# Kernel tuning notes

Hardware: AMD Instinct MI355X
Metric: run time of the kernel (lower is better)

Reference implementation:

```python
import jax, jax.numpy as jnp
import numpy as np

NUM_CAPSULE = 64
DIM_CAPSULE = 128
ROUTINGS = 3
EPS = 1e-7  # K.epsilon()


def squash(s, axis=-1):
    sq_norm = jnp.sum(jnp.square(s), axis=axis, keepdims=True) + EPS
    scale = jnp.sqrt(sq_norm) / (0.5 + sq_norm)
    return scale * s


def setup_inputs() -> dict:
    key = jax.random.key(0)
    k1, k2 = jax.random.split(key)
    B, N_IN, D_IN = 16, 512, 256
    x = jax.random.normal(k1, (B, N_IN, D_IN), dtype=jnp.float32)
    # glorot-uniform kernel (flattened conv1d kernel of shape (1, D_IN, NC*DC))
    fan_out = NUM_CAPSULE * DIM_CAPSULE
    limit = float(np.sqrt(6.0 / (D_IN + fan_out)))
    kernel = jax.random.uniform(k2, (D_IN, fan_out), dtype=jnp.float32,
                                minval=-limit, maxval=limit)
    return {"x": x, "kernel": kernel}


def reference(x, kernel):
    B, N, _ = x.shape
    # conv1d with kernel_size=1 == matmul over last dim
    hat = jnp.einsum('bni,io->bno', x, kernel)
    hat = hat.reshape(B, N, NUM_CAPSULE, DIM_CAPSULE).transpose(0, 2, 1, 3)  # [B, C, N, D]
    b = jnp.zeros((B, NUM_CAPSULE, N), dtype=hat.dtype)
    o = None
    for i in range(ROUTINGS):
        c = jax.nn.softmax(b, axis=1)  # softmax over output capsules (axis 1)
        o = squash(jnp.einsum('bcn,bcnd->bcd', c, hat))  # [B, C, D]
        if i < ROUTINGS - 1:
            b = b + jnp.einsum('bcd,bcnd->bcn', o, hat)
    return o
```

## Files before the change

### kernel.cpp

```cpp
#include <hip/hip_runtime.h>
#include <hip/hip_bf16.h>

#define NB 16
#define NN 512
#define DI 256
#define NC 64
#define ND 128
#define FO 8192
#define NP 16

typedef __attribute__((ext_vector_type(8))) short short8v;
typedef __attribute__((ext_vector_type(4))) short short4v;
typedef __attribute__((ext_vector_type(4))) float f32x4;
typedef unsigned short us16;

__device__ __forceinline__ us16 f2b(float f) {
  union { __hip_bfloat16 h; us16 u; } cv; cv.h = __float2bfloat16(f); return cv.u;
}
__device__ __forceinline__ float b2f(us16 u) {
  union { unsigned u; float f; } cv; cv.u = ((unsigned)u) << 16; return cv.f;
}

__global__ __launch_bounds__(256) void k_pre(const float* __restrict__ x,
                                             const float* __restrict__ kern,
                                             us16* __restrict__ khT,
                                             us16* __restrict__ kh,
                                             us16* __restrict__ xh,
                                             us16* __restrict__ xhT,
                                             float* __restrict__ xsum_p) {
  int task = blockIdx.x;
  int tid = threadIdx.x;

  if (task < 512) {
    int c = task >> 3, i0 = (task & 7) * 32;
    __shared__ float buf[32][129];
#pragma unroll
    for (int k = 0; k < 4; ++k) {
      int e4 = tid + k * 256;
      int r = e4 >> 5, dq = e4 & 31;
      float4 v = *(const float4*)(kern + (size_t)(i0 + r) * FO + c * ND + dq * 4);
      buf[r][dq * 4 + 0] = v.x; buf[r][dq * 4 + 1] = v.y;
      buf[r][dq * 4 + 2] = v.z; buf[r][dq * 4 + 3] = v.w;
    }
    __syncthreads();
#pragma unroll
    for (int k = 0; k < 16; ++k) {
      int e = tid + k * 256;
      int il = e & 31, d = e >> 5;
      khT[((size_t)c * ND + d) * DI + i0 + il] = f2b(buf[il][d]);
    }
  } else if (task < 1024) {
    int idx = task - 512;
    int b = idx >> 5, rem = idx & 31;
    int nb = (rem >> 2) * 64, ib = (rem & 3) * 64;
    __shared__ float buf2[64][68];
#pragma unroll
    for (int k = 0; k < 4; ++k) {
      int e4 = tid + k * 256;
      int nl = e4 >> 4, q4 = e4 & 15;
      float4 v = *(const float4*)(x + ((size_t)b * NN + nb + nl) * DI + ib + q4 * 4);
      *(float4*)&buf2[nl][q4 * 4] = v;
    }
    __syncthreads();
    {
      int nl = tid >> 2, ig = (tid & 3) * 16;
      us16 tmp[16];
#pragma unroll
      for (int e = 0; e < 16; ++e) tmp[e] = f2b(buf2[nl][ig + e]);
      us16* dst = xh + ((size_t)b * NN + nb + nl) * DI + ib + ig;
      *(short8v*)dst = *(short8v*)tmp;
      *(short8v*)(dst + 8) = *(short8v*)(tmp + 8);
    }
    {
      int il = tid & 63, ng = tid >> 6;
      us16 tmp[16];
#pragma unroll
      for (int e = 0; e < 16; ++e) tmp[e] = f2b(buf2[ng * 16 + e][il]);
      us16* dst = xhT + ((size_t)b * DI + ib + il) * NN + nb + ng * 16;
      *(short8v*)dst = *(short8v*)tmp;
      *(short8v*)(dst + 8) = *(short8v*)(tmp + 8);
    }
  } else if (task < 1088) {
    int idx = task - 1024;
    int b = idx >> 2, q = idx & 3;
    int ns = tid >> 6, i4 = tid & 63;
    float4 a = {0.f, 0.f, 0.f, 0.f};
    const float4* xp = (const float4*)(x + ((size_t)b * NN + q * 128 + ns * 32) * DI) + i4;
#pragma unroll 4
    for (int n = 0; n < 32; ++n) {
      float4 v = xp[(size_t)n * 64];
      a.x += v.x; a.y += v.y; a.z += v.z; a.w += v.w;
    }
    __shared__ float4 red[4][64];
    red[ns][i4] = a;
    __syncthreads();
    if (ns == 0) {
      float4 s0 = red[0][i4], s1 = red[1][i4], s2 = red[2][i4], s3 = red[3][i4];
      float4 s;
      s.x = s0.x + s1.x + s2.x + s3.x;  s.y = s0.y + s1.y + s2.y + s3.y;
      s.z = s0.z + s1.z + s2.z + s3.z;  s.w = s0.w + s1.w + s2.w + s3.w;
      ((float4*)(xsum_p + ((size_t)q * NB + b) * DI))[i4] = s;
    }
  } else {
    int blk2 = task - 1088;
#pragma unroll
    for (int t = 0; t < 16; ++t) {
      size_t e = (size_t)blk2 * 16384 + (size_t)t * 1024 + (size_t)tid * 4;
      float4 v = *(const float4*)(kern + e);
      us16 tmp[4] = {f2b(v.x), f2b(v.y), f2b(v.z), f2b(v.w)};
      *(short4v*)(kh + e) = *(short4v*)tmp;
    }
  }
}

template <bool FIRST>
__global__ __launch_bounds__(256) void k_owm(const us16* __restrict__ khT,
                                             const us16* __restrict__ kh,
                                             const us16* __restrict__ yp_in,
                                             const float* __restrict__ xsum_p,
                                             us16* __restrict__ whc) {
  int c = blockIdx.x, b0 = blockIdx.y * 4;
  int tid = threadIdx.x;
  int lane = tid & 63, w = tid >> 6;
  int m16 = lane & 15, ko = lane >> 4;

  __shared__ us16 ybf[16][DI];
  __shared__ float o_f32[4][ND];
  __shared__ us16 ob[4][ND];

  {
    int bb = tid >> 6, i4 = tid & 63;
    float4 v;
    if constexpr (FIRST) {
      float4 s0 = ((const float4*)(xsum_p + ((size_t)0 * NB + b0 + bb) * DI))[i4];
      float4 s1 = ((const float4*)(xsum_p + ((size_t)1 * NB + b0 + bb) * DI))[i4];
      float4 s2 = ((const float4*)(xsum_p + ((size_t)2 * NB + b0 + bb) * DI))[i4];
      float4 s3 = ((const float4*)(xsum_p + ((size_t)3 * NB + b0 + bb) * DI))[i4];
      v.x = (s0.x + s1.x + s2.x + s3.x) * (1.f / 64.f);
      v.y = (s0.y + s1.y + s2.y + s3.y) * (1.f / 64.f);
      v.z = (s0.z + s1.z + s2.z + s3.z) * (1.f / 64.f);
      v.w = (s0.w + s1.w + s2.w + s3.w) * (1.f / 64.f);
    } else {
      float a0 = 0.f, a1 = 0.f, a2 = 0.f, a3 = 0.f;
      const us16* base = yp_in + ((size_t)(b0 + bb) * NC + c) * DI + i4 * 4;
#pragma unroll
      for (int p = 0; p < NP; ++p) {
        short4v t = *(const short4v*)(base + (size_t)p * (NB * NC * DI));
        a0 += b2f((us16)t[0]); a1 += b2f((us16)t[1]);
        a2 += b2f((us16)t[2]); a3 += b2f((us16)t[3]);
      }
      v.x = a0; v.y = a1; v.z = a2; v.w = a3;
    }
    us16 tmp[4] = {f2b(v.x), f2b(v.y), f2b(v.z), f2b(v.w)};
    *(short4v*)&ybf[bb][i4 * 4] = *(short4v*)tmp;
#pragma unroll
    for (int r = 0; r < 12; ++r) ybf[4 + r][tid] = 0;
  }
  __syncthreads();

  {
#pragma unroll
    for (int nt = 0; nt < 2; ++nt) {
      int d0 = (w * 2 + nt) * 16;
      f32x4 acc = {0.f, 0.f, 0.f, 0.f};
#pragma unroll
      for (int kk = 0; kk < 8; ++kk) {
        short8v av = *(const short8v*)&ybf[m16][kk * 32 + ko * 8];
        short8v bv = *(const short8v*)(khT + ((size_t)c * ND + d0 + m16) * DI + kk * 32 + ko * 8);
        acc = __builtin_amdgcn_mfma_f32_16x16x32_bf16(av, bv, acc, 0, 0, 0);
      }
      if (ko == 0) {
#pragma unroll
        for (int r = 0; r < 4; ++r) o_f32[r][d0 + m16] = acc[r];
      }
    }
  }
  __syncthreads();

  if (tid < 128) {
    int bb = tid >> 5, j = tid & 31;
    float4 o = *(const float4*)&o_f32[bb][j * 4];
    float sq = o.x * o.x + o.y * o.y + o.z * o.z + o.w * o.w;
#pragma unroll
    for (int off = 16; off >= 1; off >>= 1) sq += __shfl_xor(sq, off, 64);
    float tot = sq + 1e-7f;
    float scale = sqrtf(tot) / (0.5f + tot);
    us16 tmp[4] = {f2b(o.x * scale), f2b(o.y * scale), f2b(o.z * scale), f2b(o.w * scale)};
    *(short4v*)&ob[bb][j * 4] = *(short4v*)tmp;
  }
  __syncthreads();

  {
#pragma unroll
    for (int nt = 0; nt < 4; ++nt) {
      int i0 = (w * 4 + nt) * 16;
      f32x4 acc = {0.f, 0.f, 0.f, 0.f};
#pragma unroll
      for (int kk = 0; kk < 4; ++kk) {
        short8v av = *(const short8v*)&ob[m16 & 3][kk * 32 + ko * 8];
        short8v bv = *(const short8v*)(kh + (size_t)(i0 + m16) * FO + c * ND + kk * 32 + ko * 8);
        acc = __builtin_amdgcn_mfma_f32_16x16x32_bf16(av, bv, acc, 0, 0, 0);
      }
      if (ko == 0) {
#pragma unroll
        for (int r = 0; r < 4; ++r)
          whc[((size_t)(b0 + r) * NC + c) * DI + i0 + m16] = f2b(acc[r]);
      }
    }
  }
}

template <bool ADD_B, bool STORE_B>
__global__ __launch_bounds__(512) void k_sy(const us16* __restrict__ xh,
                                            const us16* __restrict__ xhT,
                                            const us16* __restrict__ whc,
                                            float* __restrict__ blog,
                                            us16* __restrict__ y_p) {
  int b = blockIdx.x, p = blockIdx.y;
  int tid = threadIdx.x;
  int lane = tid & 63, w = tid >> 6;
  int m16 = lane & 15, ko = lane >> 4;

  __shared__ float s_lds[32][65];
  __shared__ us16 cT[64][40];

  int n0 = p * 32;

  {
    int Mt = w & 3, Nt = w >> 2;
    const us16* wrow = whc + ((size_t)b * NC + Mt * 16 + m16) * DI + ko * 8;
    const us16* xrow = xh + ((size_t)b * NN + n0 + Nt * 16 + m16) * DI + ko * 8;
    f32x4 acc = {0.f, 0.f, 0.f, 0.f};
#pragma unroll
    for (int k8 = 0; k8 < 8; ++k8) {
      short8v av = *(const short8v*)(wrow + k8 * 32);
      short8v bv = *(const short8v*)(xrow + k8 * 32);
      acc = __builtin_amdgcn_mfma_f32_16x16x32_bf16(av, bv, acc, 0, 0, 0);
    }
#pragma unroll
    for (int r = 0; r < 4; ++r)
      s_lds[Nt * 16 + m16][Mt * 16 + ko * 4 + r] = acc[r];
  }
  __syncthreads();

  {
    us16 pk[4];
#pragma unroll
    for (int nn = 0; nn < 4; ++nn) {
      int n = w * 4 + nn;
      float v = s_lds[n][lane];
      size_t gi = ((size_t)b * NN + n0 + n) * NC + lane;
      if (ADD_B) v += blog[gi];
      if (STORE_B) blog[gi] = v;
      float m = v;
#pragma unroll
      for (int off = 32; off >= 1; off >>= 1) m = fmaxf(m, __shfl_xor(m, off, 64));
      float e = __expf(v - m);
      float s = e;
#pragma unroll
      for (int off = 32; off >= 1; off >>= 1) s += __shfl_xor(s, off, 64);
      pk[nn] = f2b(e / s);
    }
    *(short4v*)&cT[lane][w * 4] = *(short4v*)pk;
  }
  __syncthreads();

  {
    int Mp = w >> 2, Ng = w & 3;
    short8v a0 = *(const short8v*)&cT[(Mp * 2 + 0) * 16 + m16][ko * 8];
    short8v a1 = *(const short8v*)&cT[(Mp * 2 + 1) * 16 + m16][ko * 8];
    f32x4 acc[2][4];
#pragma unroll
    for (int t = 0; t < 2; ++t)
#pragma unroll
      for (int q = 0; q < 4; ++q) { acc[t][q][0]=acc[t][q][1]=acc[t][q][2]=acc[t][q][3]=0.f; }
#pragma unroll
    for (int q = 0; q < 4; ++q) {
      int icol = (Ng * 4 + q) * 16 + m16;
      short8v bv = *(const short8v*)(xhT + ((size_t)b * DI + icol) * NN + n0 + ko * 8);
      acc[0][q] = __builtin_amdgcn_mfma_f32_16x16x32_bf16(a0, bv, acc[0][q], 0, 0, 0);
      acc[1][q] = __builtin_amdgcn_mfma_f32_16x16x32_bf16(a1, bv, acc[1][q], 0, 0, 0);
    }
    us16* yb = y_p + ((size_t)p * NB + b) * (NC * DI);
#pragma unroll
    for (int t = 0; t < 2; ++t)
#pragma unroll
      for (int q = 0; q < 4; ++q)
#pragma unroll
        for (int r = 0; r < 4; ++r)
          yb[(size_t)((Mp * 2 + t) * 16 + ko * 4 + r) * DI + (Ng * 4 + q) * 16 + m16] =
              f2b(acc[t][q][r]);
  }
}

__global__ __launch_bounds__(256) void k_of(const float* __restrict__ kern,
                                            const us16* __restrict__ yp_in,
                                            float* __restrict__ outp) {
  int c = blockIdx.x, b0 = blockIdx.y * 4;
  int tid = threadIdx.x;
  __shared__ float y_lds[4][DI];
  __shared__ f32x4 p_lds[8][4][32];

  {
    int bb = tid >> 6, i4 = tid & 63;
    float a0 = 0.f, a1 = 0.f, a2 = 0.f, a3 = 0.f;
    const us16* base = yp_in + ((size_t)(b0 + bb) * NC + c) * DI + i4 * 4;
#pragma unroll
    for (int p = 0; p < NP; ++p) {
      short4v t = *(const short4v*)(base + (size_t)p * (NB * NC * DI));
      a0 += b2f((us16)t[0]); a1 += b2f((us16)t[1]);
      a2 += b2f((us16)t[2]); a3 += b2f((us16)t[3]);
    }
    float4 v = {a0, a1, a2, a3};
    *(float4*)&y_lds[bb][i4 * 4] = v;
  }
  __syncthreads();

  {
    int dq = tid & 31, h = tid >> 5;
    f32x4 acc[4];
#pragma unroll
    for (int bb = 0; bb < 4; ++bb) { acc[bb][0]=acc[bb][1]=acc[bb][2]=acc[bb][3]=0.f; }
    const float* kp = kern + c * ND + dq * 4;
#pragma unroll 2
    for (int t = 0; t < 32; t += 4) {
      int i = h * 32 + t;
      float4 kv0 = *(const float4*)(kp + (size_t)(i + 0) * FO);
      float4 kv1 = *(const float4*)(kp + (size_t)(i + 1) * FO);
      float4 kv2 = *(const float4*)(kp + (size_t)(i + 2) * FO);
      float4 kv3 = *(const float4*)(kp + (size_t)(i + 3) * FO);
#pragma unroll
      for (int bb = 0; bb < 4; ++bb) {
        float4 yv = *(const float4*)&y_lds[bb][i];
        acc[bb][0] += yv.x * kv0.x + yv.y * kv1.x + yv.z * kv2.x + yv.w * kv3.x;
        acc[bb][1] += yv.x * kv0.y + yv.y * kv1.y + yv.z * kv2.y + yv.w * kv3.y;
        acc[bb][2] += yv.x * kv0.z + yv.y * kv1.z + yv.z * kv2.z + yv.w * kv3.z;
        acc[bb][3] += yv.x * kv0.w + yv.y * kv1.w + yv.z * kv2.w + yv.w * kv3.w;
      }
    }
#pragma unroll
    for (int bb = 0; bb < 4; ++bb) p_lds[h][bb][dq] = acc[bb];
  }
  __syncthreads();

  if (tid < 128) {
    int bb = tid >> 5, j = tid & 31;
    f32x4 o = {0.f, 0.f, 0.f, 0.f};
#pragma unroll
    for (int h = 0; h < 8; ++h) {
      f32x4 p = p_lds[h][bb][j];
      o[0] += p[0]; o[1] += p[1]; o[2] += p[2]; o[3] += p[3];
    }
    float sq = o[0]*o[0] + o[1]*o[1] + o[2]*o[2] + o[3]*o[3];
#pragma unroll
    for (int off = 16; off >= 1; off >>= 1) sq += __shfl_xor(sq, off, 64);
    float tot = sq + 1e-7f;
    float scale = sqrtf(tot) / (0.5f + tot);
    float4 st = {o[0] * scale, o[1] * scale, o[2] * scale, o[3] * scale};
    ((float4*)(outp + ((size_t)(b0 + bb) * NC + c) * ND))[j] = st;
  }
}

extern "C" void kernel_launch(void* const* d_in, const int* in_sizes, int n_in,
                              void* d_out, int out_size, void* d_ws, size_t ws_size,
                              hipStream_t stream) {
  (void)in_sizes; (void)n_in; (void)out_size; (void)ws_size;
  const float* x    = (const float*)d_in[0];
  const float* kern = (const float*)d_in[1];
  float* out = (float*)d_out;

  char* wp = (char*)d_ws;
  us16* khT  = (us16*)wp;  wp += (size_t)NC * ND * DI * 2;
  us16* kh   = (us16*)wp;  wp += (size_t)DI * FO * 2;
  us16* xh   = (us16*)wp;  wp += (size_t)NB * NN * DI * 2;
  us16* xhT  = (us16*)wp;  wp += (size_t)NB * DI * NN * 2;
  us16* whc  = (us16*)wp;  wp += (size_t)NB * NC * DI * 2;
  us16* y_p  = (us16*)wp;  wp += (size_t)NP * NB * NC * DI * 2;
  float* blog   = (float*)wp;  wp += (size_t)NB * NN * NC * 4;
  float* xsum_p = (float*)wp;

  k_pre<<<1216, 256, 0, stream>>>(x, kern, khT, kh, xh, xhT, xsum_p);

  k_owm<true><<<dim3(NC, 4), 256, 0, stream>>>(khT, kh, y_p, xsum_p, whc);
  k_sy<false, true><<<dim3(NB, NP), 512, 0, stream>>>(xh, xhT, whc, blog, y_p);
  k_owm<false><<<dim3(NC, 4), 256, 0, stream>>>(khT, kh, y_p, xsum_p, whc);
  k_sy<true, false><<<dim3(NB, NP), 512, 0, stream>>>(xh, xhT, whc, blog, y_p);
  k_of<<<dim3(NC, 4), 256, 0, stream>>>(kern, y_p, out);
}
```

Before: 61.04 us.

## Batch all 16 batches per capsule block, halve partials, fuse final squash into MFMA kernel

k_owm now handles all 16 batches in one 512-thread block per capsule. This fills the MFMA M dimension with real rows instead of zero padding and reads khT/kh once per capsule instead of four times. It also uses XOR-swizzled LDS for the y and o operands. The final fp32 scalar k_of kernel is replaced by a third k_owm mode that computes o with bf16 MFMA and writes the squashed output directly. k_sy processes 64 tokens per block with NP reduced to 8, halving the partial-sum buffers the next stage must reduce, and the separate kh conversion path is folded into the khT transpose tasks of k_pre. The trade-offs are fewer blocks per launch and bf16 precision in the final projection.

```diff
diff --git a/kernel.cpp b/kernel.cpp
--- a/kernel.cpp
+++ b/kernel.cpp
@@ -7,7 +7,7 @@
 #define NC 64
 #define ND 128
 #define FO 8192
-#define NP 16
+#define NP 8
 
 typedef __attribute__((ext_vector_type(8))) short short8v;
 typedef __attribute__((ext_vector_type(4))) short short4v;
@@ -49,6 +49,15 @@
       int il = e & 31, d = e >> 5;
       khT[((size_t)c * ND + d) * DI + i0 + il] = f2b(buf[il][d]);
     }
+    {
+      int r = tid >> 3, dg = (tid & 7) * 16;
+      us16 tmp[16];
+#pragma unroll
+      for (int e = 0; e < 16; ++e) tmp[e] = f2b(buf[r][dg + e]);
+      us16* dst = kh + (size_t)(i0 + r) * FO + c * ND + dg;
+      *(short8v*)dst = *(short8v*)tmp;
+      *(short8v*)(dst + 8) = *(short8v*)(tmp + 8);
+    }
   } else if (task < 1024) {
     int idx = task - 512;
     int b = idx >> 5, rem = idx & 31;
@@ -80,7 +89,7 @@
       *(short8v*)dst = *(short8v*)tmp;
       *(short8v*)(dst + 8) = *(short8v*)(tmp + 8);
     }
-  } else if (task < 1088) {
+  } else {
     int idx = task - 1024;
     int b = idx >> 2, q = idx & 3;
     int ns = tid >> 6, i4 = tid & 63;
@@ -101,111 +110,106 @@
       s.z = s0.z + s1.z + s2.z + s3.z;  s.w = s0.w + s1.w + s2.w + s3.w;
       ((float4*)(xsum_p + ((size_t)q * NB + b) * DI))[i4] = s;
     }
-  } else {
-    int blk2 = task - 1088;
-#pragma unroll
-    for (int t = 0; t < 16; ++t) {
-      size_t e = (size_t)blk2 * 16384 + (size_t)t * 1024 + (size_t)tid * 4;
-      float4 v = *(const float4*)(kern + e);
-      us16 tmp[4] = {f2b(v.x), f2b(v.y), f2b(v.z), f2b(v.w)};
-      *(short4v*)(kh + e) = *(short4v*)tmp;
-    }
-  }
-}
-
-template <bool FIRST>
-__global__ __launch_bounds__(256) void k_owm(const us16* __restrict__ khT,
+  }
+}
+
+template <int MODE>
+__global__ __launch_bounds__(512) void k_owm(const us16* __restrict__ khT,
                                              const us16* __restrict__ kh,
                                              const us16* __restrict__ yp_in,
                                              const float* __restrict__ xsum_p,
-                                             us16* __restrict__ whc) {
-  int c = blockIdx.x, b0 = blockIdx.y * 4;
+                                             us16* __restrict__ whc,
+                                             float* __restrict__ outp) {
+  int c = blockIdx.x;
   int tid = threadIdx.x;
   int lane = tid & 63, w = tid >> 6;
   int m16 = lane & 15, ko = lane >> 4;
 
-  __shared__ us16 ybf[16][DI];
-  __shared__ float o_f32[4][ND];
-  __shared__ us16 ob[4][ND];
-
-  {
-    int bb = tid >> 6, i4 = tid & 63;
-    float4 v;
-    if constexpr (FIRST) {
-      float4 s0 = ((const float4*)(xsum_p + ((size_t)0 * NB + b0 + bb) * DI))[i4];
-      float4 s1 = ((const float4*)(xsum_p + ((size_t)1 * NB + b0 + bb) * DI))[i4];
-      float4 s2 = ((const float4*)(xsum_p + ((size_t)2 * NB + b0 + bb) * DI))[i4];
-      float4 s3 = ((const float4*)(xsum_p + ((size_t)3 * NB + b0 + bb) * DI))[i4];
-      v.x = (s0.x + s1.x + s2.x + s3.x) * (1.f / 64.f);
-      v.y = (s0.y + s1.y + s2.y + s3.y) * (1.f / 64.f);
-      v.z = (s0.z + s1.z + s2.z + s3.z) * (1.f / 64.f);
-      v.w = (s0.w + s1.w + s2.w + s3.w) * (1.f / 64.f);
+  __shared__ us16 ybf[16 * 256];
+  __shared__ us16 ob[16 * 128];
+  __shared__ float o_f32[16][132];
+
+  {
+    int b = tid >> 5, u = tid & 31;
+    int i8 = u * 8;
+    float v[8];
+#pragma unroll
+    for (int e = 0; e < 8; ++e) v[e] = 0.f;
+    if constexpr (MODE == 0) {
+#pragma unroll
+      for (int q = 0; q < 4; ++q) {
+        const float* sp = xsum_p + ((size_t)q * NB + b) * DI + i8;
+        float4 a = *(const float4*)sp;
+        float4 d = *(const float4*)(sp + 4);
+        v[0] += a.x; v[1] += a.y; v[2] += a.z; v[3] += a.w;
+        v[4] += d.x; v[5] += d.y; v[6] += d.z; v[7] += d.w;
+      }
+#pragma unroll
+      for (int e = 0; e < 8; ++e) v[e] *= (1.f / 64.f);
     } else {
-      float a0 = 0.f, a1 = 0.f, a2 = 0.f, a3 = 0.f;
-      const us16* base = yp_in + ((size_t)(b0 + bb) * NC + c) * DI + i4 * 4;
+      const us16* base = yp_in + ((size_t)b * NC + c) * DI + i8;
 #pragma unroll
       for (int p = 0; p < NP; ++p) {
-        short4v t = *(const short4v*)(base + (size_t)p * (NB * NC * DI));
-        a0 += b2f((us16)t[0]); a1 += b2f((us16)t[1]);
-        a2 += b2f((us16)t[2]); a3 += b2f((us16)t[3]);
+        short8v t = *(const short8v*)(base + (size_t)p * (NB * NC * DI));
+#pragma unroll
+        for (int e = 0; e < 8; ++e) v[e] += b2f((us16)t[e]);
       }
-      v.x = a0; v.y = a1; v.z = a2; v.w = a3;
-    }
-    us16 tmp[4] = {f2b(v.x), f2b(v.y), f2b(v.z), f2b(v.w)};
-    *(short4v*)&ybf[bb][i4 * 4] = *(short4v*)tmp;
-#pragma unroll
-    for (int r = 0; r < 12; ++r) ybf[4 + r][tid] = 0;
-  }
-  __syncthreads();
-
-  {
-#pragma unroll
-    for (int nt = 0; nt < 2; ++nt) {
-      int d0 = (w * 2 + nt) * 16;
-      f32x4 acc = {0.f, 0.f, 0.f, 0.f};
-#pragma unroll
-      for (int kk = 0; kk < 8; ++kk) {
-        short8v av = *(const short8v*)&ybf[m16][kk * 32 + ko * 8];
-        short8v bv = *(const short8v*)(khT + ((size_t)c * ND + d0 + m16) * DI + kk * 32 + ko * 8);
-        acc = __builtin_amdgcn_mfma_f32_16x16x32_bf16(av, bv, acc, 0, 0, 0);
-      }
-      if (ko == 0) {
-#pragma unroll
-        for (int r = 0; r < 4; ++r) o_f32[r][d0 + m16] = acc[r];
-      }
-    }
-  }
-  __syncthreads();
-
-  if (tid < 128) {
-    int bb = tid >> 5, j = tid & 31;
-    float4 o = *(const float4*)&o_f32[bb][j * 4];
+    }
+    us16 tmp[8];
+#pragma unroll
+    for (int e = 0; e < 8; ++e) tmp[e] = f2b(v[e]);
+    *(short8v*)&ybf[b * 256 + ((u ^ (b & 7)) * 8)] = *(short8v*)tmp;
+  }
+  __syncthreads();
+
+  {
+    int d0 = w * 16;
+    f32x4 acc = {0.f, 0.f, 0.f, 0.f};
+#pragma unroll
+    for (int kk = 0; kk < 8; ++kk) {
+      int kb = kk * 4 + ko;
+      short8v av = *(const short8v*)&ybf[m16 * 256 + ((kb ^ (m16 & 7)) * 8)];
+      short8v bv = *(const short8v*)(khT + ((size_t)c * ND + d0 + m16) * DI + kk * 32 + ko * 8);
+      acc = __builtin_amdgcn_mfma_f32_16x16x32_bf16(av, bv, acc, 0, 0, 0);
+    }
+#pragma unroll
+    for (int r = 0; r < 4; ++r) o_f32[ko * 4 + r][d0 + m16] = acc[r];
+  }
+  __syncthreads();
+
+  {
+    int b = tid >> 5, j = tid & 31;
+    float4 o = *(const float4*)&o_f32[b][j * 4];
     float sq = o.x * o.x + o.y * o.y + o.z * o.z + o.w * o.w;
 #pragma unroll
     for (int off = 16; off >= 1; off >>= 1) sq += __shfl_xor(sq, off, 64);
     float tot = sq + 1e-7f;
     float scale = sqrtf(tot) / (0.5f + tot);
-    us16 tmp[4] = {f2b(o.x * scale), f2b(o.y * scale), f2b(o.z * scale), f2b(o.w * scale)};
-    *(short4v*)&ob[bb][j * 4] = *(short4v*)tmp;
-  }
-  __syncthreads();
-
-  {
-#pragma unroll
-    for (int nt = 0; nt < 4; ++nt) {
-      int i0 = (w * 4 + nt) * 16;
+    o.x *= scale; o.y *= scale; o.z *= scale; o.w *= scale;
+    if constexpr (MODE == 2) {
+      ((float4*)(outp + ((size_t)b * NC + c) * ND))[j] = o;
+    } else {
+      us16 tmp[4] = {f2b(o.x), f2b(o.y), f2b(o.z), f2b(o.w)};
+      *(short4v*)&ob[b * 128 + (((j >> 1) ^ (b & 7)) * 8) + (j & 1) * 4] = *(short4v*)tmp;
+    }
+  }
+  __syncthreads();
+
+  if constexpr (MODE < 2) {
+#pragma unroll
+    for (int nt = 0; nt < 2; ++nt) {
+      int i0 = (w * 2 + nt) * 16;
       f32x4 acc = {0.f, 0.f, 0.f, 0.f};
 #pragma unroll
       for (int kk = 0; kk < 4; ++kk) {
-        short8v av = *(const short8v*)&ob[m16 & 3][kk * 32 + ko * 8];
+        int kb = kk * 4 + ko;
+        short8v av = *(const short8v*)&ob[m16 * 128 + ((kb ^ (m16 & 7)) * 8)];
         short8v bv = *(const short8v*)(kh + (size_t)(i0 + m16) * FO + c * ND + kk * 32 + ko * 8);
         acc = __builtin_amdgcn_mfma_f32_16x16x32_bf16(av, bv, acc, 0, 0, 0);
       }
-      if (ko == 0) {
-#pragma unroll
-        for (int r = 0; r < 4; ++r)
-          whc[((size_t)(b0 + r) * NC + c) * DI + i0 + m16] = f2b(acc[r]);
-      }
+#pragma unroll
+      for (int r = 0; r < 4; ++r)
+        whc[((size_t)(ko * 4 + r) * NC + c) * DI + i0 + m16] = f2b(acc[r]);
     }
   }
 }
@@ -220,34 +224,37 @@
   int tid = threadIdx.x;
   int lane = tid & 63, w = tid >> 6;
   int m16 = lane & 15, ko = lane >> 4;
-
-  __shared__ float s_lds[32][65];
-  __shared__ us16 cT[64][40];
-
-  int n0 = p * 32;
-
-  {
-    int Mt = w & 3, Nt = w >> 2;
-    const us16* wrow = whc + ((size_t)b * NC + Mt * 16 + m16) * DI + ko * 8;
-    const us16* xrow = xh + ((size_t)b * NN + n0 + Nt * 16 + m16) * DI + ko * 8;
-    f32x4 acc = {0.f, 0.f, 0.f, 0.f};
-#pragma unroll
-    for (int k8 = 0; k8 < 8; ++k8) {
-      short8v av = *(const short8v*)(wrow + k8 * 32);
-      short8v bv = *(const short8v*)(xrow + k8 * 32);
-      acc = __builtin_amdgcn_mfma_f32_16x16x32_bf16(av, bv, acc, 0, 0, 0);
-    }
-#pragma unroll
-    for (int r = 0; r < 4; ++r)
-      s_lds[Nt * 16 + m16][Mt * 16 + ko * 4 + r] = acc[r];
-  }
-  __syncthreads();
-
-  {
-    us16 pk[4];
-#pragma unroll
-    for (int nn = 0; nn < 4; ++nn) {
-      int n = w * 4 + nn;
+  int n0 = p * 64;
+
+  __shared__ float s_lds[64][65];
+  __shared__ us16 cT[64][72];
+
+  {
+    int Mt = w & 3;
+#pragma unroll
+    for (int t = 0; t < 2; ++t) {
+      int Nt = (w >> 2) * 2 + t;
+      const us16* wrow = whc + ((size_t)b * NC + Mt * 16 + m16) * DI + ko * 8;
+      const us16* xrow = xh + ((size_t)b * NN + n0 + Nt * 16 + m16) * DI + ko * 8;
+      f32x4 acc = {0.f, 0.f, 0.f, 0.f};
+#pragma unroll
+      for (int k8 = 0; k8 < 8; ++k8) {
+        short8v av = *(const short8v*)(wrow + k8 * 32);
+        short8v bv = *(const short8v*)(xrow + k8 * 32);
+        acc = __builtin_amdgcn_mfma_f32_16x16x32_bf16(av, bv, acc, 0, 0, 0);
+      }
+#pragma unroll
+      for (int r = 0; r < 4; ++r)
+        s_lds[Nt * 16 + m16][Mt * 16 + ko * 4 + r] = acc[r];
+    }
+  }
+  __syncthreads();
+
+  {
+    us16 pk[8];
+#pragma unroll
+    for (int nn = 0; nn < 8; ++nn) {
+      int n = w * 8 + nn;
       float v = s_lds[n][lane];
       size_t gi = ((size_t)b * NN + n0 + n) * NC + lane;
       if (ADD_B) v += blog[gi];
@@ -261,103 +268,28 @@
       for (int off = 32; off >= 1; off >>= 1) s += __shfl_xor(s, off, 64);
       pk[nn] = f2b(e / s);
     }
-    *(short4v*)&cT[lane][w * 4] = *(short4v*)pk;
-  }
-  __syncthreads();
-
-  {
-    int Mp = w >> 2, Ng = w & 3;
-    short8v a0 = *(const short8v*)&cT[(Mp * 2 + 0) * 16 + m16][ko * 8];
-    short8v a1 = *(const short8v*)&cT[(Mp * 2 + 1) * 16 + m16][ko * 8];
-    f32x4 acc[2][4];
-#pragma unroll
-    for (int t = 0; t < 2; ++t)
-#pragma unroll
-      for (int q = 0; q < 4; ++q) { acc[t][q][0]=acc[t][q][1]=acc[t][q][2]=acc[t][q][3]=0.f; }
-#pragma unroll
-    for (int q = 0; q < 4; ++q) {
-      int icol = (Ng * 4 + q) * 16 + m16;
-      short8v bv = *(const short8v*)(xhT + ((size_t)b * DI + icol) * NN + n0 + ko * 8);
-      acc[0][q] = __builtin_amdgcn_mfma_f32_16x16x32_bf16(a0, bv, acc[0][q], 0, 0, 0);
-      acc[1][q] = __builtin_amdgcn_mfma_f32_16x16x32_bf16(a1, bv, acc[1][q], 0, 0, 0);
-    }
+    *(short8v*)&cT[lane][w * 8] = *(short8v*)pk;
+  }
+  __syncthreads();
+
+  {
+    int Mt2 = w & 3;
+    short8v a0 = *(const short8v*)&cT[Mt2 * 16 + m16][ko * 8];
+    short8v a1 = *(const short8v*)&cT[Mt2 * 16 + m16][32 + ko * 8];
     us16* yb = y_p + ((size_t)p * NB + b) * (NC * DI);
 #pragma unroll
-    for (int t = 0; t < 2; ++t)
-#pragma unroll
-      for (int q = 0; q < 4; ++q)
-#pragma unroll
-        for (int r = 0; r < 4; ++r)
-          yb[(size_t)((Mp * 2 + t) * 16 + ko * 4 + r) * DI + (Ng * 4 + q) * 16 + m16] =
-              f2b(acc[t][q][r]);
-  }
-}
-
-__global__ __launch_bounds__(256) void k_of(const float* __restrict__ kern,
-                                            const us16* __restrict__ yp_in,
-                                            float* __restrict__ outp) {
-  int c = blockIdx.x, b0 = blockIdx.y * 4;
-  int tid = threadIdx.x;
-  __shared__ float y_lds[4][DI];
-  __shared__ f32x4 p_lds[8][4][32];
-
-  {
-    int bb = tid >> 6, i4 = tid & 63;
-    float a0 = 0.f, a1 = 0.f, a2 = 0.f, a3 = 0.f;
-    const us16* base = yp_in + ((size_t)(b0 + bb) * NC + c) * DI + i4 * 4;
-#pragma unroll
-    for (int p = 0; p < NP; ++p) {
-      short4v t = *(const short4v*)(base + (size_t)p * (NB * NC * DI));
-      a0 += b2f((us16)t[0]); a1 += b2f((us16)t[1]);
-      a2 += b2f((us16)t[2]); a3 += b2f((us16)t[3]);
-    }
-    float4 v = {a0, a1, a2, a3};
-    *(float4*)&y_lds[bb][i4 * 4] = v;
-  }
-  __syncthreads();
-
-  {
-    int dq = tid & 31, h = tid >> 5;
-    f32x4 acc[4];
-#pragma unroll
-    for (int bb = 0; bb < 4; ++bb) { acc[bb][0]=acc[bb][1]=acc[bb][2]=acc[bb][3]=0.f; }
-    const float* kp = kern + c * ND + dq * 4;
-#pragma unroll 2
-    for (int t = 0; t < 32; t += 4) {
-      int i = h * 32 + t;
-      float4 kv0 = *(const float4*)(kp + (size_t)(i + 0) * FO);
-      float4 kv1 = *(const float4*)(kp + (size_t)(i + 1) * FO);
-      float4 kv2 = *(const float4*)(kp + (size_t)(i + 2) * FO);
-      float4 kv3 = *(const float4*)(kp + (size_t)(i + 3) * FO);
-#pragma unroll
-      for (int bb = 0; bb < 4; ++bb) {
-        float4 yv = *(const float4*)&y_lds[bb][i];
-        acc[bb][0] += yv.x * kv0.x + yv.y * kv1.x + yv.z * kv2.x + yv.w * kv3.x;
-        acc[bb][1] += yv.x * kv0.y + yv.y * kv1.y + yv.z * kv2.y + yv.w * kv3.y;
-        acc[bb][2] += yv.x * kv0.z + yv.y * kv1.z + yv.z * kv2.z + yv.w * kv3.z;
-        acc[bb][3] += yv.x * kv0.w + yv.y * kv1.w + yv.z * kv2.w + yv.w * kv3.w;
-      }
-    }
-#pragma unroll
-    for (int bb = 0; bb < 4; ++bb) p_lds[h][bb][dq] = acc[bb];
-  }
-  __syncthreads();
-
-  if (tid < 128) {
-    int bb = tid >> 5, j = tid & 31;
-    f32x4 o = {0.f, 0.f, 0.f, 0.f};
-#pragma unroll
-    for (int h = 0; h < 8; ++h) {
-      f32x4 p = p_lds[h][bb][j];
-      o[0] += p[0]; o[1] += p[1]; o[2] += p[2]; o[3] += p[3];
-    }
-    float sq = o[0]*o[0] + o[1]*o[1] + o[2]*o[2] + o[3]*o[3];
-#pragma unroll
-    for (int off = 16; off >= 1; off >>= 1) sq += __shfl_xor(sq, off, 64);
-    float tot = sq + 1e-7f;
-    float scale = sqrtf(tot) / (0.5f + tot);
-    float4 st = {o[0] * scale, o[1] * scale, o[2] * scale, o[3] * scale};
-    ((float4*)(outp + ((size_t)(b0 + bb) * NC + c) * ND))[j] = st;
+    for (int q = 0; q < 8; ++q) {
+      int it = (w >> 2) * 8 + q;
+      const us16* xr = xhT + ((size_t)b * DI + it * 16 + m16) * NN + n0;
+      f32x4 acc = {0.f, 0.f, 0.f, 0.f};
+      short8v bv0 = *(const short8v*)(xr + ko * 8);
+      short8v bv1 = *(const short8v*)(xr + 32 + ko * 8);
+      acc = __builtin_amdgcn_mfma_f32_16x16x32_bf16(a0, bv0, acc, 0, 0, 0);
+      acc = __builtin_amdgcn_mfma_f32_16x16x32_bf16(a1, bv1, acc, 0, 0, 0);
+#pragma unroll
+      for (int r = 0; r < 4; ++r)
+        yb[(size_t)(Mt2 * 16 + ko * 4 + r) * DI + it * 16 + m16] = f2b(acc[r]);
+    }
   }
 }
 
@@ -379,11 +311,11 @@
   float* blog   = (float*)wp;  wp += (size_t)NB * NN * NC * 4;
   float* xsum_p = (float*)wp;
 
-  k_pre<<<1216, 256, 0, stream>>>(x, kern, khT, kh, xh, xhT, xsum_p);
-
-  k_owm<true><<<dim3(NC, 4), 256, 0, stream>>>(khT, kh, y_p, xsum_p, whc);
+  k_pre<<<1088, 256, 0, stream>>>(x, kern, khT, kh, xh, xhT, xsum_p);
+
+  k_owm<0><<<NC, 512, 0, stream>>>(khT, kh, y_p, xsum_p, whc, nullptr);
   k_sy<false, true><<<dim3(NB, NP), 512, 0, stream>>>(xh, xhT, whc, blog, y_p);
-  k_owm<false><<<dim3(NC, 4), 256, 0, stream>>>(khT, kh, y_p, xsum_p, whc);
+  k_owm<1><<<NC, 512, 0, stream>>>(khT, kh, y_p, xsum_p, whc, nullptr);
   k_sy<true, false><<<dim3(NB, NP), 512, 0, stream>>>(xh, xhT, whc, blog, y_p);
-  k_of<<<dim3(NC, 4), 256, 0, stream>>>(kern, y_p, out);
-}
+  k_owm<2><<<NC, 512, 0, stream>>>(khT, kh, y_p, xsum_p, whc, out);
+}
```

Result: slower. 63.55 us (+4.1%).
